# Performance work log

Hardware: AMD Instinct MI355X
Metric: run time of the kernel (lower is better)

## Reference

```python
import jax, jax.numpy as jnp
import numpy as np

NUM_HEADS = 32
HEAD_DIM = 128
HIDDEN = NUM_HEADS * HEAD_DIM  # 4096
ROPE_BASE = 10000.0
VISION_TOKEN_TYPE = 1


def vision_expert_mask(token_type_ids):
    # vision_token_mask[:, :-1] = (tt[:, :-1]==1) & (tt[:, 1:]==1); last col False
    tt = token_type_ids
    m = (tt[:, :-1] == VISION_TOKEN_TYPE) & (tt[:, 1:] == VISION_TOKEN_TYPE)
    return jnp.concatenate([m, jnp.zeros((tt.shape[0], 1), dtype=bool)], axis=1)


def rotary_cos_sin(position_ids, head_dim, dtype):
    inv_freq = 1.0 / (ROPE_BASE ** (jnp.arange(0, head_dim, 2, dtype=jnp.float32) / head_dim))
    freqs = position_ids.astype(jnp.float32)[..., None] * inv_freq  # [B,S,Dh/2]
    emb = jnp.concatenate([freqs, freqs], axis=-1)  # [B,S,Dh]
    return jnp.cos(emb).astype(dtype), jnp.sin(emb).astype(dtype)


def rotate_half(x):
    d = x.shape[-1] // 2
    return jnp.concatenate([-x[..., d:], x[..., :d]], axis=-1)


def setup_inputs() -> dict:
    key = jax.random.key(0)
    ks = jax.random.split(key, 5)
    B, S = 2, 2048
    hidden_states = jax.random.normal(ks[0], (B, S, HIDDEN), dtype=jnp.float32)
    token_type_ids = jax.random.randint(ks[1], (B, S), 0, 2, dtype=jnp.int64)
    position_ids = jnp.broadcast_to(jnp.arange(S, dtype=jnp.int64)[None, :], (B, S))
    scale = 0.02
    w_vis_qkv = jax.random.normal(ks[2], (HIDDEN, 3 * HIDDEN), dtype=jnp.float32) * scale
    w_lang_qkv = jax.random.normal(ks[3], (HIDDEN, 3 * HIDDEN), dtype=jnp.float32) * scale
    w_vis_dense = jax.random.normal(ks[4], (HIDDEN, HIDDEN), dtype=jnp.float32) * scale
    w_lang_dense = jax.random.normal(jax.random.fold_in(key, 7), (HIDDEN, HIDDEN), dtype=jnp.float32) * scale
    return dict(hidden_states=hidden_states, token_type_ids=token_type_ids,
                position_ids=position_ids, w_vis_qkv=w_vis_qkv, w_lang_qkv=w_lang_qkv,
                w_vis_dense=w_vis_dense, w_lang_dense=w_lang_dense)


def reference(hidden_states, token_type_ids, position_ids,
              w_vis_qkv, w_lang_qkv, w_vis_dense, w_lang_dense):
    B, S, D = hidden_states.shape
    vm = vision_expert_mask(token_type_ids)  # [B,S] bool

    # 2-expert QKV dispatch (mask-select between the two expert GEMMs)
    qkv = jnp.where(vm[..., None],
                    hidden_states @ w_vis_qkv,
                    hidden_states @ w_lang_qkv)  # [B,S,3D]
    q, k, v = jnp.split(qkv, 3, axis=-1)
    q = q.reshape(B, S, NUM_HEADS, HEAD_DIM)
    k = k.reshape(B, S, NUM_HEADS, HEAD_DIM)
    v = v.reshape(B, S, NUM_HEADS, HEAD_DIM)

    # rotary embedding on q, k
    cos, sin = rotary_cos_sin(position_ids, HEAD_DIM, q.dtype)  # [B,S,Dh]
    cos, sin = cos[:, :, None, :], sin[:, :, None, :]
    q = q * cos + rotate_half(q) * sin
    k = k * cos + rotate_half(k) * sin

    # causal attention (dense equivalent of the paged-attention call)
    scores = jnp.einsum('bqhd,bkhd->bhqk', q, k) / jnp.sqrt(jnp.array(HEAD_DIM, q.dtype))
    causal = jnp.tril(jnp.ones((S, S), dtype=bool))
    scores = jnp.where(causal[None, None], scores, jnp.finfo(scores.dtype).min)
    probs = jax.nn.softmax(scores, axis=-1)
    ctx = jnp.einsum('bhqk,bkhd->bqhd', probs, v).reshape(B, S, D)

    # 2-expert output dense dispatch
    attn_output = jnp.where(vm[..., None],
                            ctx @ w_vis_dense,
                            ctx @ w_lang_dense)
    return attn_output
```

## Files before the change

### kernel.cpp

```cpp
#include <hip/hip_runtime.h>
#include <math.h>

#define SEQ     2048
#define NB      2
#define NHEADS  32
#define DHEAD   128
#define HID     4096
#define NQKV    12288
#define T_TOKENS (NB*SEQ)

typedef _Float16 half8 __attribute__((ext_vector_type(8)));
typedef float v4f __attribute__((ext_vector_type(4)));

__device__ __forceinline__ void gload_lds16(const void* g, void* l) {
    __builtin_amdgcn_global_load_lds(
        (__attribute__((address_space(1))) void*)(void*)(g),
        (__attribute__((address_space(3))) void*)(unsigned)(unsigned long long)(l),
        16, 0, 0);
}

__device__ __forceinline__ v4f mfma16(half8 a, half8 b, v4f c) {
    return __builtin_amdgcn_mfma_f32_16x16x32_f16(a, b, c, 0, 0, 0);
}

__global__ void route_kernel(const int* __restrict__ tt, int* counts, int* idx) {
    int t = blockIdx.x * blockDim.x + threadIdx.x;
    if (t >= T_TOKENS) return;
    int s = t & (SEQ - 1);
    bool vm = (s < SEQ - 1) && (tt[t] == 1) && (tt[t + 1] == 1);
    int e = vm ? 0 : 1;
    int p = atomicAdd(&counts[e], 1);
    idx[e * T_TOKENS + p] = t;
}

__global__ void rope_table_kernel(const int* __restrict__ pos_ids, float2* __restrict__ tab) {
    int i = blockIdx.x * blockDim.x + threadIdx.x;
    if (i >= T_TOKENS * 64) return;
    int tok = i >> 6, j = i & 63;
    float invf = (float)pow(10000.0, -(double)j * (1.0 / 64.0));
    float ang = (float)pos_ids[tok] * invf;
    double ds, dc;
    sincos((double)ang, &ds, &dc);
    tab[i] = make_float2((float)dc, (float)ds);
}

__global__ void cvt_f32_f16(const float* __restrict__ src, _Float16* __restrict__ dst, int n4) {
    int i = blockIdx.x * blockDim.x + threadIdx.x;
    if (i >= n4) return;
    float4 v = ((const float4*)src)[i];
    union { _Float16 h[4]; uint2 u; } p;
    p.h[0] = (_Float16)v.x; p.h[1] = (_Float16)v.y;
    p.h[2] = (_Float16)v.z; p.h[3] = (_Float16)v.w;
    ((uint2*)dst)[i] = p.u;
}

__global__ void transpose_cvt(const float* __restrict__ W, _Float16* __restrict__ WT,
                              int K, int N) {
    __shared__ _Float16 t[64][72];
    const int n0 = blockIdx.x * 64, k0 = blockIdx.y * 64;
    const int cr = threadIdx.x & 15, rr = threadIdx.x >> 4;
#pragma unroll
    for (int it = 0; it < 4; ++it) {
        int r = rr + it * 16;
        float4 v = *(const float4*)&W[(size_t)(k0 + r) * N + n0 + cr * 4];
        t[cr*4+0][r] = (_Float16)v.x; t[cr*4+1][r] = (_Float16)v.y;
        t[cr*4+2][r] = (_Float16)v.z; t[cr*4+3][r] = (_Float16)v.w;
    }
    __syncthreads();
#pragma unroll
    for (int it = 0; it < 4; ++it) {
        int r = rr + it * 16;
        union { _Float16 h[4]; uint2 u; } p;
#pragma unroll
        for (int j = 0; j < 4; ++j) p.h[j] = t[r][cr*4+j];
        *(uint2*)&WT[(size_t)(n0 + r) * K + k0 + cr * 4] = p.u;
    }
}

__global__ void transpose_v(const _Float16* __restrict__ vin, _Float16* __restrict__ vout) {
    __shared__ _Float16 t[64][72];
    const int s0 = blockIdx.x * 64;
    const int d0 = blockIdx.y * 64;
    const int bh = blockIdx.z;
    const int b = bh >> 5, h = bh & 31;
    const int cr = threadIdx.x & 15, rr = threadIdx.x >> 4;
#pragma unroll
    for (int it = 0; it < 4; ++it) {
        int sl = rr + it * 16;
        union { _Float16 h4[4]; uint2 u; } p;
        p.u = *(const uint2*)&vin[(size_t)(b * SEQ + s0 + sl) * HID + h * DHEAD + d0 + cr * 4];
#pragma unroll
        for (int j = 0; j < 4; ++j) t[cr*4+j][sl] = p.h4[j];
    }
    __syncthreads();
#pragma unroll
    for (int it = 0; it < 4; ++it) {
        int dl = rr + it * 16;
        union { _Float16 h4[4]; uint2 u; } p;
#pragma unroll
        for (int j = 0; j < 4; ++j) p.h4[j] = t[dl][cr*4+j];
        *(uint2*)&vout[((size_t)bh * DHEAD + d0 + dl) * SEQ + s0 + cr * 4] = p.u;
    }
}

template <int MODE, int NCT>
__global__ __launch_bounds__(512, 2)
void gemm_expert(const _Float16* __restrict__ A,
                 const _Float16* __restrict__ BT0,
                 const _Float16* __restrict__ BT1,
                 const int* __restrict__ counts,
                 const int* __restrict__ idx_all,
                 const float2* __restrict__ rope,
                 _Float16* __restrict__ qbuf,
                 _Float16* __restrict__ kbuf,
                 _Float16* __restrict__ vbuf,
                 float* __restrict__ out) {
    const int e = blockIdx.z;
    const int count = counts[e];

    const int f   = blockIdx.x + NCT * blockIdx.y;
    const int xcd = f & 7;
    const int g   = f >> 3;
    const int c   = g >> 5;
    const int wi  = g & 31;
    const int rt  = wi >> 1;
    const int ct  = xcd * (NCT / 8) + c * 2 + (wi & 1);

    if (rt * 256 >= count) return;
    const int* idx = idx_all + e * T_TOKENS;
    const _Float16* BT = e ? BT1 : BT0;

    __shared__ _Float16 sA[4][256 * 32];
    __shared__ _Float16 sB[4][256 * 32];

    const int tid = threadIdx.x;
    const int w = tid >> 6, lane = tid & 63;
    const int col = lane & 15, quad = lane >> 4;
    const int wm = w >> 2, wn = w & 3;

    const int schk = (lane & 3) ^ ((lane >> 3) & 3);
    const _Float16* ag[2];
    const _Float16* bg[2];
    int so[2];
#pragma unroll
    for (int o = 0; o < 2; ++o) {
        int r = w * 32 + o * 16 + (lane >> 2);
        int gg = rt * 256 + r; if (gg > count - 1) gg = count - 1;
        ag[o] = A + (size_t)idx[gg] * HID + schk * 8;
        bg[o] = BT + (size_t)(ct * 256 + r) * HID + schk * 8;
        so[o] = (w * 32 + o * 16) * 32;
    }

    v4f acc[8][4];
#pragma unroll
    for (int i = 0; i < 8; ++i)
#pragma unroll
        for (int j = 0; j < 4; ++j) { v4f z = {0.f, 0.f, 0.f, 0.f}; acc[i][j] = z; }

    const int kofq = (quad ^ ((col >> 1) & 3)) * 8;

    auto stage = [&](int buf) {
#pragma unroll
        for (int o = 0; o < 2; ++o) {
            gload_lds16(ag[o], &sA[buf][so[o]]);
            gload_lds16(bg[o], &sB[buf][so[o]]);
            ag[o] += 32; bg[o] += 32;
        }
    };
    auto compute = [&](int cur) {
        half8 a[8], b[4];
#pragma unroll
        for (int i = 0; i < 8; ++i)
            a[i] = *(const half8*)&sA[cur][(wm * 128 + i * 16 + col) * 32 + kofq];
#pragma unroll
        for (int j = 0; j < 4; ++j)
            b[j] = *(const half8*)&sB[cur][((4 * j + wn) * 16 + col) * 32 + kofq];
#pragma unroll
        for (int i = 0; i < 8; ++i)
#pragma unroll
            for (int j = 0; j < 4; ++j)
                acc[i][j] = mfma16(a[i], b[j], acc[i][j]);
    };

    const int NK = HID / 32;
    stage(0); stage(1); stage(2);

    for (int kt = 0; kt < NK - 3; ++kt) {
        asm volatile("s_waitcnt vmcnt(8)" ::: "memory");
        __builtin_amdgcn_s_barrier();
        asm volatile("" ::: "memory");
        stage((kt + 3) & 3);
        compute(kt & 3);
    }
    asm volatile("s_waitcnt vmcnt(8)" ::: "memory");
    __builtin_amdgcn_s_barrier();
    asm volatile("" ::: "memory");
    compute((NK - 3) & 3);
    asm volatile("s_waitcnt vmcnt(4)" ::: "memory");
    __builtin_amdgcn_s_barrier();
    asm volatile("" ::: "memory");
    compute((NK - 2) & 3);
    asm volatile("s_waitcnt vmcnt(0)" ::: "memory");
    __builtin_amdgcn_s_barrier();
    asm volatile("" ::: "memory");
    compute((NK - 1) & 3);

    const int n0 = ct * 256;
    if (MODE == 1) {
#pragma unroll
        for (int i = 0; i < 8; ++i)
#pragma unroll
            for (int r = 0; r < 4; ++r) {
                int rg = rt * 256 + wm * 128 + i * 16 + quad * 4 + r;
                if (rg >= count) continue;
                int tok = idx[rg];
                float* dst = out + (size_t)tok * HID + n0;
#pragma unroll
                for (int j = 0; j < 4; ++j) dst[(4 * j + wn) * 16 + col] = acc[i][j][r];
            }
    } else {
        const int sec = n0 >> 12;
        const int h0 = (n0 >> 7) & 31;
#pragma unroll
        for (int i = 0; i < 8; ++i)
#pragma unroll
            for (int r = 0; r < 4; ++r) {
                int rg = rt * 256 + wm * 128 + i * 16 + quad * 4 + r;
                if (rg >= count) continue;
                int tok = idx[rg];
                int b = tok >> 11, s = tok & (SEQ - 1);
                if (sec == 2) {
#pragma unroll
                    for (int j = 0; j < 4; ++j) {
                        int h = (h0 + (j >> 1)) & 31;
                        vbuf[(size_t)tok * HID + h * DHEAD + (j & 1) * 64 + wn * 16 + col] =
                            (_Float16)acc[i][j][r];
                    }
                } else {
                    const float2* tp = rope + (size_t)tok * 64;
                    int d = wn * 16 + col;
                    float2 cs = tp[d];
#pragma unroll
                    for (int jj = 0; jj < 4; jj += 2) {
                        int h = (h0 + (jj >> 1)) & 31;
                        _Float16* dst = (sec ? kbuf : qbuf) +
                            ((size_t)(b * NHEADS + h) * SEQ + s) * DHEAD;
                        float x = acc[i][jj][r], y = acc[i][jj + 1][r];
                        dst[d]      = (_Float16)(x * cs.x - y * cs.y);
                        dst[d + 64] = (_Float16)(y * cs.x + x * cs.y);
                    }
                }
            }
    }
}

__global__ __launch_bounds__(256, 2)
void attn_kernel(const _Float16* __restrict__ qbuf,
                 const _Float16* __restrict__ kbuf,
                 const _Float16* __restrict__ vt,
                 _Float16* __restrict__ ctx) {
    const int f   = blockIdx.x;
    const int xcd = f & 7;
    const int t   = f >> 3;
    const int s   = t & 31;
    const int rr  = t >> 5;
    const int u   = s & 15, g = s >> 4;
    const int bh  = xcd * 8 + rr * 2 + g;
    const int qt  = (rr & 1) ? (15 - u) : u;

    const int b = bh >> 5, h = bh & 31;
    const int tid = threadIdx.x;
    const int w = tid >> 6, lane = tid & 63;
    const int col = lane & 15, quad = lane >> 4;

    __shared__ _Float16 sK[2][64 * 128];
    __shared__ _Float16 sV[2][128 * 64];
    __shared__ _Float16 sP[128 * 64];

    half8 qf[2][4];
    const _Float16 qscale = (_Float16)0.08838834764831845f;
#pragma unroll
    for (int mt = 0; mt < 2; ++mt)
#pragma unroll
        for (int kc = 0; kc < 4; ++kc) {
            int row = qt * 128 + w * 32 + mt * 16 + col;
            half8 v = *(const half8*)&qbuf[((size_t)bh * SEQ + row) * DHEAD + kc * 32 + quad * 8];
            qf[mt][kc] = v * qscale;
        }

    float mrow[2][4], lrow[2][4];
    v4f o[2][8];
#pragma unroll
    for (int mt = 0; mt < 2; ++mt)
#pragma unroll
        for (int r = 0; r < 4; ++r) { mrow[mt][r] = -3.0e38f; lrow[mt][r] = 0.f; }
#pragma unroll
    for (int i = 0; i < 2; ++i)
#pragma unroll
        for (int j = 0; j < 8; ++j) { v4f z = {0.f, 0.f, 0.f, 0.f}; o[i][j] = z; }

    const int cxor = col & 7;
    const int vs_chk = (lane & 7) ^ (lane >> 3);
    const int nkt = 2 * qt + 2;

    const _Float16* kg0 = kbuf + (size_t)bh * SEQ * DHEAD;
    const _Float16* vg0 = vt + (size_t)bh * DHEAD * SEQ;

    auto stage = [&](int kt, int buf) {
        const _Float16* kg = kg0 + (size_t)kt * 64 * DHEAD;
        const _Float16* vg = vg0 + kt * 64;
#pragma unroll
        for (int op = 0; op < 4; ++op) {
            int r0 = (w * 4 + op) * 4;
            int krow = r0 + quad;
            int kcs = col ^ (krow & 7);
            gload_lds16(kg + (size_t)krow * DHEAD + kcs * 8, &sK[buf][r0 * 128]);
            int d0 = (w * 4 + op) * 8;
            int vrow = d0 + (lane >> 3);
            gload_lds16(vg + (size_t)vrow * SEQ + vs_chk * 8, &sV[buf][d0 * 64]);
        }
    };

    stage(0, 0);
    __syncthreads();

    for (int kt = 0; kt < nkt; ++kt) {
        const int cur = kt & 1;
        if (kt + 1 < nkt) stage(kt + 1, cur ^ 1);

        v4f sc[2][4];
#pragma unroll
        for (int i = 0; i < 2; ++i)
#pragma unroll
            for (int j = 0; j < 4; ++j) { v4f z = {0.f, 0.f, 0.f, 0.f}; sc[i][j] = z; }
        __builtin_amdgcn_s_setprio(1);
#pragma unroll
        for (int kc = 0; kc < 4; ++kc) {
            const int kof = ((kc * 4 + quad) ^ cxor) * 8;
#pragma unroll
            for (int nt = 0; nt < 4; ++nt) {
                half8 bf = *(const half8*)&sK[cur][(size_t)(nt * 16 + col) * 128 + kof];
                sc[0][nt] = mfma16(qf[0][kc], bf, sc[0][nt]);
                sc[1][nt] = mfma16(qf[1][kc], bf, sc[1][nt]);
            }
        }
        __builtin_amdgcn_s_setprio(0);

        if (kt >= 2 * qt) {
#pragma unroll
            for (int mt = 0; mt < 2; ++mt)
#pragma unroll
                for (int nt = 0; nt < 4; ++nt)
#pragma unroll
                    for (int r = 0; r < 4; ++r) {
                        int rowa = qt * 128 + w * 32 + mt * 16 + quad * 4 + r;
                        int cola = kt * 64 + nt * 16 + col;
                        if (cola > rowa) sc[mt][nt][r] = -3.0e38f;
                    }
        }

#pragma unroll
        for (int mt = 0; mt < 2; ++mt)
#pragma unroll
            for (int r = 0; r < 4; ++r) {
                float mx = sc[mt][0][r];
#pragma unroll
                for (int nt = 1; nt < 4; ++nt) mx = fmaxf(mx, sc[mt][nt][r]);
                mx = fmaxf(mx, __shfl_xor(mx, 1));
                mx = fmaxf(mx, __shfl_xor(mx, 2));
                mx = fmaxf(mx, __shfl_xor(mx, 4));
                mx = fmaxf(mx, __shfl_xor(mx, 8));
                float newm = fmaxf(mrow[mt][r], mx);
                float alpha = __expf(mrow[mt][r] - newm);
                mrow[mt][r] = newm;
                float rs = 0.f;
#pragma unroll
                for (int nt = 0; nt < 4; ++nt) {
                    float p = __expf(sc[mt][nt][r] - newm);
                    sc[mt][nt][r] = p;
                    rs += p;
                }
                rs += __shfl_xor(rs, 1); rs += __shfl_xor(rs, 2);
                rs += __shfl_xor(rs, 4); rs += __shfl_xor(rs, 8);
                lrow[mt][r] = lrow[mt][r] * alpha + rs;
#pragma unroll
                for (int nt = 0; nt < 8; ++nt) o[mt][nt][r] *= alpha;
            }

#pragma unroll
        for (int mt = 0; mt < 2; ++mt)
#pragma unroll
            for (int nt = 0; nt < 4; ++nt)
#pragma unroll
                for (int r = 0; r < 4; ++r) {
                    int rp = w * 32 + mt * 16 + quad * 4 + r;
                    int colh = nt * 16 + col;
                    int c = (colh >> 3) ^ (rp & 7);
                    sP[(size_t)rp * 64 + c * 8 + (colh & 7)] = (_Float16)sc[mt][nt][r];
                }

        __builtin_amdgcn_s_setprio(1);
#pragma unroll
        for (int kc = 0; kc < 2; ++kc) {
            const int kof = ((kc * 4 + quad) ^ cxor) * 8;
            half8 p0 = *(const half8*)&sP[(size_t)(w * 32 + col) * 64 + kof];
            half8 p1 = *(const half8*)&sP[(size_t)(w * 32 + 16 + col) * 64 + kof];
#pragma unroll
            for (int nt = 0; nt < 8; ++nt) {
                half8 vf = *(const half8*)&sV[cur][(size_t)(nt * 16 + col) * 64 + kof];
                o[0][nt] = mfma16(p0, vf, o[0][nt]);
                o[1][nt] = mfma16(p1, vf, o[1][nt]);
            }
        }
        __builtin_amdgcn_s_setprio(0);

        __syncthreads();
    }

#pragma unroll
    for (int mt = 0; mt < 2; ++mt)
#pragma unroll
        for (int r = 0; r < 4; ++r) {
            int rowa = qt * 128 + w * 32 + mt * 16 + quad * 4 + r;
            float inv = 1.0f / lrow[mt][r];
            _Float16* dst = ctx + ((size_t)b * SEQ + rowa) * HID + h * DHEAD;
#pragma unroll
            for (int nt = 0; nt < 8; ++nt)
                dst[nt * 16 + col] = (_Float16)(o[mt][nt][r] * inv);
        }
}

extern "C" void kernel_launch(void* const* d_in, const int* in_sizes, int n_in,
                              void* d_out, int out_size, void* d_ws, size_t ws_size,
                              hipStream_t stream) {
    const float* hidden = (const float*)d_in[0];
    const int*   tt     = (const int*)d_in[1];
    const int*   pos    = (const int*)d_in[2];
    const float* wvq    = (const float*)d_in[3];
    const float* wlq    = (const float*)d_in[4];
    const float* wvd    = (const float*)d_in[5];
    const float* wld    = (const float*)d_in[6];
    float* out = (float*)d_out;

    char* ws = (char*)d_ws;
    size_t off = 0;
    auto alloc = [&](size_t bytes) {
        char* p = ws + off;
        off += (bytes + 255) & ~(size_t)255;
        return p;
    };
    const size_t TOKB = (size_t)T_TOKENS * HID * sizeof(_Float16);
    _Float16* h16  = (_Float16*)alloc(TOKB);
    _Float16* wvqT = (_Float16*)alloc((size_t)NQKV * HID * 2);
    _Float16* wlqT = (_Float16*)alloc((size_t)NQKV * HID * 2);
    _Float16* wvdT = (_Float16*)alloc((size_t)HID * HID * 2);
    _Float16* wldT = (_Float16*)alloc((size_t)HID * HID * 2);
    _Float16* qb   = (_Float16*)alloc(TOKB);
    _Float16* kb   = (_Float16*)alloc(TOKB);
    _Float16* vtmp = (_Float16*)alloc(TOKB);
    int* counts = (int*)alloc(2 * sizeof(int));
    int* idx    = (int*)alloc(2 * T_TOKENS * sizeof(int));
    float2* rope = (float2*)alloc((size_t)T_TOKENS * 64 * sizeof(float2));
    _Float16* vT  = h16;
    _Float16* ctx = vtmp;

    hipMemsetAsync(counts, 0, 2 * sizeof(int), stream);
    route_kernel<<<T_TOKENS / 256, 256, 0, stream>>>(tt, counts, idx);
    rope_table_kernel<<<(T_TOKENS * 64) / 256, 256, 0, stream>>>(pos, rope);
    cvt_f32_f16<<<(T_TOKENS * HID / 4) / 256, 256, 0, stream>>>(hidden, h16, T_TOKENS * HID / 4);
    transpose_cvt<<<dim3(NQKV / 64, HID / 64), 256, 0, stream>>>(wvq, wvqT, HID, NQKV);
    transpose_cvt<<<dim3(NQKV / 64, HID / 64), 256, 0, stream>>>(wlq, wlqT, HID, NQKV);
    transpose_cvt<<<dim3(HID / 64, HID / 64), 256, 0, stream>>>(wvd, wvdT, HID, HID);
    transpose_cvt<<<dim3(HID / 64, HID / 64), 256, 0, stream>>>(wld, wldT, HID, HID);
    gemm_expert<0, NQKV / 256><<<dim3(NQKV / 256, T_TOKENS / 256, 2), 512, 0, stream>>>(
        h16, wvqT, wlqT, counts, idx, rope, qb, kb, vtmp, nullptr);
    transpose_v<<<dim3(SEQ / 64, DHEAD / 64, NB * NHEADS), 256, 0, stream>>>(vtmp, vT);
    attn_kernel<<<dim3(16 * NB * NHEADS), 256, 0, stream>>>(qb, kb, vT, ctx);
    gemm_expert<1, HID / 256><<<dim3(HID / 256, T_TOKENS / 256, 2), 512, 0, stream>>>(
        ctx, wvdT, wldT, counts, idx, nullptr, nullptr, nullptr, nullptr, out);
}
```

Before: 1.535 ms.

## Enlarge attention query tile to 256 rows and use 128-tile GEMM for output projection

The attention kernel now processes 256 query rows per block with 512 threads, so each staged K/V tile is shared by twice as many query rows. Warps skip compute on fully masked key tiles but still join the barriers. A new 128x128-tile expert GEMM with a 4-stage global-to-LDS pipeline replaces the 256-tile one for the output dense projection, giving more blocks for better CU fill on the smaller N=4096 problem. The larger attention blocks cut occupancy and worsen causal load imbalance, since warps idle on skipped tiles.

Result: faster. 1.499 ms (-2.3%).

```diff
diff --git a/kernel.cpp b/kernel.cpp
--- a/kernel.cpp
+++ b/kernel.cpp
@@ -105,16 +105,16 @@
 
 template <int MODE, int NCT>
 __global__ __launch_bounds__(512, 2)
-void gemm_expert(const _Float16* __restrict__ A,
-                 const _Float16* __restrict__ BT0,
-                 const _Float16* __restrict__ BT1,
-                 const int* __restrict__ counts,
-                 const int* __restrict__ idx_all,
-                 const float2* __restrict__ rope,
-                 _Float16* __restrict__ qbuf,
-                 _Float16* __restrict__ kbuf,
-                 _Float16* __restrict__ vbuf,
-                 float* __restrict__ out) {
+void gemm_expert256(const _Float16* __restrict__ A,
+                    const _Float16* __restrict__ BT0,
+                    const _Float16* __restrict__ BT1,
+                    const int* __restrict__ counts,
+                    const int* __restrict__ idx_all,
+                    const float2* __restrict__ rope,
+                    _Float16* __restrict__ qbuf,
+                    _Float16* __restrict__ kbuf,
+                    _Float16* __restrict__ vbuf,
+                    float* __restrict__ out) {
     const int e = blockIdx.z;
     const int count = counts[e];
 
@@ -254,7 +254,147 @@
     }
 }
 
+template <int MODE, int NCT>
 __global__ __launch_bounds__(256, 2)
+void gemm_expert128(const _Float16* __restrict__ A,
+                    const _Float16* __restrict__ BT0,
+                    const _Float16* __restrict__ BT1,
+                    const int* __restrict__ counts,
+                    const int* __restrict__ idx_all,
+                    const float2* __restrict__ rope,
+                    _Float16* __restrict__ qbuf,
+                    _Float16* __restrict__ kbuf,
+                    _Float16* __restrict__ vbuf,
+                    float* __restrict__ out) {
+    const int e = blockIdx.z;
+    const int count = counts[e];
+
+    const int f   = blockIdx.x + NCT * blockIdx.y;
+    const int xcd = f & 7;
+    const int g   = f >> 3;
+    const int c   = g >> 6;
+    const int wi  = g & 63;
+    const int rt  = wi >> 1;
+    const int ct  = xcd * (NCT / 8) + c * 2 + (wi & 1);
+
+    if (rt * 128 >= count) return;
+    const int* idx = idx_all + e * T_TOKENS;
+    const _Float16* BT = e ? BT1 : BT0;
+
+    __shared__ _Float16 sA[4][128 * 32];
+    __shared__ _Float16 sB[4][128 * 32];
+
+    const int tid = threadIdx.x;
+    const int w = tid >> 6, lane = tid & 63;
+    const int col = lane & 15, quad = lane >> 4;
+
+    const int r0 = (w * 2 + 0) * 16 + (lane >> 2);
+    const int r1 = (w * 2 + 1) * 16 + (lane >> 2);
+    int g0 = rt * 128 + r0; if (g0 > count - 1) g0 = count - 1;
+    int g1 = rt * 128 + r1; if (g1 > count - 1) g1 = count - 1;
+    const int tok0 = idx[g0], tok1 = idx[g1];
+    const int schk = (lane & 3) ^ ((lane >> 3) & 3);
+    const _Float16* ag0 = A + (size_t)tok0 * HID + schk * 8;
+    const _Float16* ag1 = A + (size_t)tok1 * HID + schk * 8;
+    const _Float16* bg0 = BT + (size_t)(ct * 128 + r0) * HID + schk * 8;
+    const _Float16* bg1 = BT + (size_t)(ct * 128 + r1) * HID + schk * 8;
+    const int sa_off0 = (w * 2 + 0) * 512;
+    const int sa_off1 = (w * 2 + 1) * 512;
+
+    v4f acc[2][8];
+#pragma unroll
+    for (int i = 0; i < 2; ++i)
+#pragma unroll
+        for (int j = 0; j < 8; ++j) { v4f z = {0.f, 0.f, 0.f, 0.f}; acc[i][j] = z; }
+
+    const int kofq = (quad ^ ((col >> 1) & 3)) * 8;
+    const int am0 = (w * 32 + col) * 32 + kofq;
+    const int am1 = am0 + 16 * 32;
+
+    auto stage = [&](int buf) {
+        gload_lds16(ag0, &sA[buf][sa_off0]); gload_lds16(ag1, &sA[buf][sa_off1]);
+        gload_lds16(bg0, &sB[buf][sa_off0]); gload_lds16(bg1, &sB[buf][sa_off1]);
+        ag0 += 32; ag1 += 32; bg0 += 32; bg1 += 32;
+    };
+    auto compute = [&](int cur) {
+        half8 a0 = *(const half8*)&sA[cur][am0];
+        half8 a1 = *(const half8*)&sA[cur][am1];
+#pragma unroll
+        for (int nt = 0; nt < 8; ++nt) {
+            half8 b = *(const half8*)&sB[cur][(nt * 16 + col) * 32 + kofq];
+            acc[0][nt] = mfma16(a0, b, acc[0][nt]);
+            acc[1][nt] = mfma16(a1, b, acc[1][nt]);
+        }
+    };
+
+    const int NK = HID / 32;
+    stage(0); stage(1); stage(2);
+
+    for (int kt = 0; kt < NK - 3; ++kt) {
+        asm volatile("s_waitcnt vmcnt(8)" ::: "memory");
+        __builtin_amdgcn_s_barrier();
+        asm volatile("" ::: "memory");
+        stage((kt + 3) & 3);
+        compute(kt & 3);
+    }
+    asm volatile("s_waitcnt vmcnt(8)" ::: "memory");
+    __builtin_amdgcn_s_barrier();
+    asm volatile("" ::: "memory");
+    compute((NK - 3) & 3);
+    asm volatile("s_waitcnt vmcnt(4)" ::: "memory");
+    __builtin_amdgcn_s_barrier();
+    asm volatile("" ::: "memory");
+    compute((NK - 2) & 3);
+    asm volatile("s_waitcnt vmcnt(0)" ::: "memory");
+    __builtin_amdgcn_s_barrier();
+    asm volatile("" ::: "memory");
+    compute((NK - 1) & 3);
+
+    const int n0 = ct * 128;
+    if (MODE == 1) {
+#pragma unroll
+        for (int mt = 0; mt < 2; ++mt)
+#pragma unroll
+            for (int r = 0; r < 4; ++r) {
+                int rg = rt * 128 + w * 32 + mt * 16 + quad * 4 + r;
+                if (rg >= count) continue;
+                int tok = idx[rg];
+                float* dst = out + (size_t)tok * HID + n0;
+#pragma unroll
+                for (int nt = 0; nt < 8; ++nt) dst[nt * 16 + col] = acc[mt][nt][r];
+            }
+    } else {
+        const int sec = n0 >> 12;
+        const int h = (n0 >> 7) & 31;
+#pragma unroll
+        for (int mt = 0; mt < 2; ++mt)
+#pragma unroll
+            for (int r = 0; r < 4; ++r) {
+                int rg = rt * 128 + w * 32 + mt * 16 + quad * 4 + r;
+                if (rg >= count) continue;
+                int tok = idx[rg];
+                int b = tok >> 11, s = tok & (SEQ - 1);
+                if (sec == 2) {
+                    _Float16* dst = vbuf + (size_t)tok * HID + h * DHEAD;
+#pragma unroll
+                    for (int nt = 0; nt < 8; ++nt) dst[nt * 16 + col] = (_Float16)acc[mt][nt][r];
+                } else {
+                    _Float16* dst = (sec ? kbuf : qbuf) + ((size_t)(b * NHEADS + h) * SEQ + s) * DHEAD;
+                    const float2* tp = rope + (size_t)tok * 64;
+#pragma unroll
+                    for (int nt = 0; nt < 4; ++nt) {
+                        int d = nt * 16 + col;
+                        float2 cs = tp[d];
+                        float x = acc[mt][nt][r], y = acc[mt][nt + 4][r];
+                        dst[d]      = (_Float16)(x * cs.x - y * cs.y);
+                        dst[d + 64] = (_Float16)(y * cs.x + x * cs.y);
+                    }
+                }
+            }
+    }
+}
+
+__global__ __launch_bounds__(512, 1)
 void attn_kernel(const _Float16* __restrict__ qbuf,
                  const _Float16* __restrict__ kbuf,
                  const _Float16* __restrict__ vt,
@@ -262,11 +402,11 @@
     const int f   = blockIdx.x;
     const int xcd = f & 7;
     const int t   = f >> 3;
+    const int rr  = t >> 5;
     const int s   = t & 31;
-    const int rr  = t >> 5;
-    const int u   = s & 15, g = s >> 4;
-    const int bh  = xcd * 8 + rr * 2 + g;
-    const int qt  = (rr & 1) ? (15 - u) : u;
+    const int u   = s & 3;
+    const int bh  = xcd * 8 + (s >> 2);
+    const int qt  = rr ? (7 - u) : u;
 
     const int b = bh >> 5, h = bh & 31;
     const int tid = threadIdx.x;
@@ -275,7 +415,7 @@
 
     __shared__ _Float16 sK[2][64 * 128];
     __shared__ _Float16 sV[2][128 * 64];
-    __shared__ _Float16 sP[128 * 64];
+    __shared__ _Float16 sP[256 * 64];
 
     half8 qf[2][4];
     const _Float16 qscale = (_Float16)0.08838834764831845f;
@@ -283,7 +423,7 @@
     for (int mt = 0; mt < 2; ++mt)
 #pragma unroll
         for (int kc = 0; kc < 4; ++kc) {
-            int row = qt * 128 + w * 32 + mt * 16 + col;
+            int row = qt * 256 + w * 32 + mt * 16 + col;
             half8 v = *(const half8*)&qbuf[((size_t)bh * SEQ + row) * DHEAD + kc * 32 + quad * 8];
             qf[mt][kc] = v * qscale;
         }
@@ -301,7 +441,8 @@
 
     const int cxor = col & 7;
     const int vs_chk = (lane & 7) ^ (lane >> 3);
-    const int nkt = 2 * qt + 2;
+    const int nkt = 4 * qt + 4;
+    const int rowbase = qt * 256 + w * 32;
 
     const _Float16* kg0 = kbuf + (size_t)bh * SEQ * DHEAD;
     const _Float16* vg0 = vt + (size_t)bh * DHEAD * SEQ;
@@ -310,12 +451,12 @@
         const _Float16* kg = kg0 + (size_t)kt * 64 * DHEAD;
         const _Float16* vg = vg0 + kt * 64;
 #pragma unroll
-        for (int op = 0; op < 4; ++op) {
-            int r0 = (w * 4 + op) * 4;
+        for (int op = 0; op < 2; ++op) {
+            int r0 = (w * 2 + op) * 4;
             int krow = r0 + quad;
             int kcs = col ^ (krow & 7);
             gload_lds16(kg + (size_t)krow * DHEAD + kcs * 8, &sK[buf][r0 * 128]);
-            int d0 = (w * 4 + op) * 8;
+            int d0 = (w * 2 + op) * 8;
             int vrow = d0 + (lane >> 3);
             gload_lds16(vg + (size_t)vrow * SEQ + vs_chk * 8, &sV[buf][d0 * 64]);
         }
@@ -328,91 +469,93 @@
         const int cur = kt & 1;
         if (kt + 1 < nkt) stage(kt + 1, cur ^ 1);
 
-        v4f sc[2][4];
-#pragma unroll
-        for (int i = 0; i < 2; ++i)
-#pragma unroll
-            for (int j = 0; j < 4; ++j) { v4f z = {0.f, 0.f, 0.f, 0.f}; sc[i][j] = z; }
-        __builtin_amdgcn_s_setprio(1);
-#pragma unroll
-        for (int kc = 0; kc < 4; ++kc) {
-            const int kof = ((kc * 4 + quad) ^ cxor) * 8;
-#pragma unroll
-            for (int nt = 0; nt < 4; ++nt) {
-                half8 bf = *(const half8*)&sK[cur][(size_t)(nt * 16 + col) * 128 + kof];
-                sc[0][nt] = mfma16(qf[0][kc], bf, sc[0][nt]);
-                sc[1][nt] = mfma16(qf[1][kc], bf, sc[1][nt]);
+        if (kt * 64 <= rowbase + 31) {
+            v4f sc[2][4];
+#pragma unroll
+            for (int i = 0; i < 2; ++i)
+#pragma unroll
+                for (int j = 0; j < 4; ++j) { v4f z = {0.f, 0.f, 0.f, 0.f}; sc[i][j] = z; }
+            __builtin_amdgcn_s_setprio(1);
+#pragma unroll
+            for (int kc = 0; kc < 4; ++kc) {
+                const int kof = ((kc * 4 + quad) ^ cxor) * 8;
+#pragma unroll
+                for (int nt = 0; nt < 4; ++nt) {
+                    half8 bf = *(const half8*)&sK[cur][(size_t)(nt * 16 + col) * 128 + kof];
+                    sc[0][nt] = mfma16(qf[0][kc], bf, sc[0][nt]);
+                    sc[1][nt] = mfma16(qf[1][kc], bf, sc[1][nt]);
+                }
             }
+            __builtin_amdgcn_s_setprio(0);
+
+            if (kt * 64 + 63 > rowbase) {
+#pragma unroll
+                for (int mt = 0; mt < 2; ++mt)
+#pragma unroll
+                    for (int nt = 0; nt < 4; ++nt)
+#pragma unroll
+                        for (int r = 0; r < 4; ++r) {
+                            int rowa = rowbase + mt * 16 + quad * 4 + r;
+                            int cola = kt * 64 + nt * 16 + col;
+                            if (cola > rowa) sc[mt][nt][r] = -3.0e38f;
+                        }
+            }
+
+#pragma unroll
+            for (int mt = 0; mt < 2; ++mt)
+#pragma unroll
+                for (int r = 0; r < 4; ++r) {
+                    float mx = sc[mt][0][r];
+#pragma unroll
+                    for (int nt = 1; nt < 4; ++nt) mx = fmaxf(mx, sc[mt][nt][r]);
+                    mx = fmaxf(mx, __shfl_xor(mx, 1));
+                    mx = fmaxf(mx, __shfl_xor(mx, 2));
+                    mx = fmaxf(mx, __shfl_xor(mx, 4));
+                    mx = fmaxf(mx, __shfl_xor(mx, 8));
+                    float newm = fmaxf(mrow[mt][r], mx);
+                    float alpha = __expf(mrow[mt][r] - newm);
+                    mrow[mt][r] = newm;
+                    float rs = 0.f;
+#pragma unroll
+                    for (int nt = 0; nt < 4; ++nt) {
+                        float p = __expf(sc[mt][nt][r] - newm);
+                        sc[mt][nt][r] = p;
+                        rs += p;
+                    }
+                    rs += __shfl_xor(rs, 1); rs += __shfl_xor(rs, 2);
+                    rs += __shfl_xor(rs, 4); rs += __shfl_xor(rs, 8);
+                    lrow[mt][r] = lrow[mt][r] * alpha + rs;
+#pragma unroll
+                    for (int nt = 0; nt < 8; ++nt) o[mt][nt][r] *= alpha;
+                }
+
+#pragma unroll
+            for (int mt = 0; mt < 2; ++mt)
+#pragma unroll
+                for (int nt = 0; nt < 4; ++nt)
+#pragma unroll
+                    for (int r = 0; r < 4; ++r) {
+                        int rp = w * 32 + mt * 16 + quad * 4 + r;
+                        int colh = nt * 16 + col;
+                        int c = (colh >> 3) ^ (rp & 7);
+                        sP[(size_t)rp * 64 + c * 8 + (colh & 7)] = (_Float16)sc[mt][nt][r];
+                    }
+
+            __builtin_amdgcn_s_setprio(1);
+#pragma unroll
+            for (int kc = 0; kc < 2; ++kc) {
+                const int kof = ((kc * 4 + quad) ^ cxor) * 8;
+                half8 p0 = *(const half8*)&sP[(size_t)(w * 32 + col) * 64 + kof];
+                half8 p1 = *(const half8*)&sP[(size_t)(w * 32 + 16 + col) * 64 + kof];
+#pragma unroll
+                for (int nt = 0; nt < 8; ++nt) {
+                    half8 vf = *(const half8*)&sV[cur][(size_t)(nt * 16 + col) * 64 + kof];
+                    o[0][nt] = mfma16(p0, vf, o[0][nt]);
+                    o[1][nt] = mfma16(p1, vf, o[1][nt]);
+                }
+            }
+            __builtin_amdgcn_s_setprio(0);
         }
-        __builtin_amdgcn_s_setprio(0);
-
-        if (kt >= 2 * qt) {
-#pragma unroll
-            for (int mt = 0; mt < 2; ++mt)
-#pragma unroll
-                for (int nt = 0; nt < 4; ++nt)
-#pragma unroll
-                    for (int r = 0; r < 4; ++r) {
-                        int rowa = qt * 128 + w * 32 + mt * 16 + quad * 4 + r;
-                        int cola = kt * 64 + nt * 16 + col;
-                        if (cola > rowa) sc[mt][nt][r] = -3.0e38f;
-                    }
-        }
-
-#pragma unroll
-        for (int mt = 0; mt < 2; ++mt)
-#pragma unroll
-            for (int r = 0; r < 4; ++r) {
-                float mx = sc[mt][0][r];
-#pragma unroll
-                for (int nt = 1; nt < 4; ++nt) mx = fmaxf(mx, sc[mt][nt][r]);
-                mx = fmaxf(mx, __shfl_xor(mx, 1));
-                mx = fmaxf(mx, __shfl_xor(mx, 2));
-                mx = fmaxf(mx, __shfl_xor(mx, 4));
-                mx = fmaxf(mx, __shfl_xor(mx, 8));
-                float newm = fmaxf(mrow[mt][r], mx);
-                float alpha = __expf(mrow[mt][r] - newm);
-                mrow[mt][r] = newm;
-                float rs = 0.f;
-#pragma unroll
-                for (int nt = 0; nt < 4; ++nt) {
-                    float p = __expf(sc[mt][nt][r] - newm);
-                    sc[mt][nt][r] = p;
-                    rs += p;
-                }
-                rs += __shfl_xor(rs, 1); rs += __shfl_xor(rs, 2);
-                rs += __shfl_xor(rs, 4); rs += __shfl_xor(rs, 8);
-                lrow[mt][r] = lrow[mt][r] * alpha + rs;
-#pragma unroll
-                for (int nt = 0; nt < 8; ++nt) o[mt][nt][r] *= alpha;
-            }
-
-#pragma unroll
-        for (int mt = 0; mt < 2; ++mt)
-#pragma unroll
-            for (int nt = 0; nt < 4; ++nt)
-#pragma unroll
-                for (int r = 0; r < 4; ++r) {
-                    int rp = w * 32 + mt * 16 + quad * 4 + r;
-                    int colh = nt * 16 + col;
-                    int c = (colh >> 3) ^ (rp & 7);
-                    sP[(size_t)rp * 64 + c * 8 + (colh & 7)] = (_Float16)sc[mt][nt][r];
-                }
-
-        __builtin_amdgcn_s_setprio(1);
-#pragma unroll
-        for (int kc = 0; kc < 2; ++kc) {
-            const int kof = ((kc * 4 + quad) ^ cxor) * 8;
-            half8 p0 = *(const half8*)&sP[(size_t)(w * 32 + col) * 64 + kof];
-            half8 p1 = *(const half8*)&sP[(size_t)(w * 32 + 16 + col) * 64 + kof];
-#pragma unroll
-            for (int nt = 0; nt < 8; ++nt) {
-                half8 vf = *(const half8*)&sV[cur][(size_t)(nt * 16 + col) * 64 + kof];
-                o[0][nt] = mfma16(p0, vf, o[0][nt]);
-                o[1][nt] = mfma16(p1, vf, o[1][nt]);
-            }
-        }
-        __builtin_amdgcn_s_setprio(0);
 
         __syncthreads();
     }
@@ -421,7 +564,7 @@
     for (int mt = 0; mt < 2; ++mt)
 #pragma unroll
         for (int r = 0; r < 4; ++r) {
-            int rowa = qt * 128 + w * 32 + mt * 16 + quad * 4 + r;
+            int rowa = rowbase + mt * 16 + quad * 4 + r;
             float inv = 1.0f / lrow[mt][r];
             _Float16* dst = ctx + ((size_t)b * SEQ + rowa) * HID + h * DHEAD;
 #pragma unroll
@@ -472,10 +615,10 @@
     transpose_cvt<<<dim3(NQKV / 64, HID / 64), 256, 0, stream>>>(wlq, wlqT, HID, NQKV);
     transpose_cvt<<<dim3(HID / 64, HID / 64), 256, 0, stream>>>(wvd, wvdT, HID, HID);
     transpose_cvt<<<dim3(HID / 64, HID / 64), 256, 0, stream>>>(wld, wldT, HID, HID);
-    gemm_expert<0, NQKV / 256><<<dim3(NQKV / 256, T_TOKENS / 256, 2), 512, 0, stream>>>(
+    gemm_expert256<0, NQKV / 256><<<dim3(NQKV / 256, T_TOKENS / 256, 2), 512, 0, stream>>>(
         h16, wvqT, wlqT, counts, idx, rope, qb, kb, vtmp, nullptr);
     transpose_v<<<dim3(SEQ / 64, DHEAD / 64, NB * NHEADS), 256, 0, stream>>>(vtmp, vT);
-    attn_kernel<<<dim3(16 * NB * NHEADS), 256, 0, stream>>>(qb, kb, vT, ctx);
-    gemm_expert<1, HID / 256><<<dim3(HID / 256, T_TOKENS / 256, 2), 512, 0, stream>>>(
+    attn_kernel<<<dim3(8 * NB * NHEADS), 512, 0, stream>>>(qb, kb, vT, ctx);
+    gemm_expert128<1, HID / 128><<<dim3(HID / 128, T_TOKENS / 128, 2), 256, 0, stream>>>(
         ctx, wvdT, wldT, counts, idx, nullptr, nullptr, nullptr, nullptr, out);
 }
```
